# Kernel tuning notes

Hardware: AMD Instinct MI355X
Metric: run time of the kernel (lower is better)

## Reference

```python
import jax, jax.numpy as jnp
import numpy as np


def _conv3x3_relu(x, w, b):
    # 3x3 conv, padding 1 (SAME), NCHW / OIHW, then ReLU (Conv2d with activation=ReLU)
    y = jax.lax.conv_general_dilated(x, w, (1, 1), ((1, 1), (1, 1)),
                                     dimension_numbers=('NCHW', 'OIHW', 'NCHW'))
    return jax.nn.relu(y + b[None, :, None, None])


def _forward(features, cnn_w, cnn_b, gcn_w, gcn_b, up_w, up_b,
             deconv_w, deconv_b, pred_w, pred_b):
    # ---- CNN stack (mask_fcn1..4) ----
    x = features
    for i in range(cnn_w.shape[0]):
        x = _conv3x3_relu(x, cnn_w[i], cnn_b[i])

    B, C, H, W = x.shape
    N = H * W  # pixels = graph nodes per ROI

    # ---- cosine-similarity adjacency per sample ----
    f = x.reshape(B, C, N).transpose(0, 2, 1)          # [B, N, C] node features
    norms = jnp.linalg.norm(f, axis=-1, keepdims=True)
    fn = f / jnp.maximum(norms, 1e-8)
    A = jnp.einsum('bnc,bmc->bnm', fn, fn)             # [B, N, N]

    # ---- symmetric GCN normalization with self-loops: D^-1/2 (A+I) D^-1/2 ----
    A = A + jnp.eye(N, dtype=A.dtype)[None]
    d = jnp.sum(A, axis=-1)                            # [B, N]
    dinv = jax.lax.rsqrt(jnp.maximum(d, 1e-12))
    A = A * dinv[:, :, None] * dinv[:, None, :]

    # ---- GCN layers: x' = A_hat @ (x W) + b, then GELU ----
    g = f
    for i in range(gcn_w.shape[0]):
        g = jnp.einsum('bnm,bmc->bnc', A, g @ gcn_w[i]) + gcn_b[i]
        g = jax.nn.gelu(g, approximate=False)

    x = g.transpose(0, 2, 1).reshape(B, C, H, W)

    # ---- Upsample head ----
    for i in range(up_w.shape[0]):
        x = _conv3x3_relu(x, up_w[i], up_b[i])
    feats = x  # returned roi_features, [B, C, H, W]

    # ConvTranspose2d(k=2, s=2): dilated conv with flipped, IO-swapped kernel
    wt = jnp.flip(deconv_w, (2, 3)).transpose(1, 0, 2, 3)  # (out, in, 2, 2)
    y = jax.lax.conv_general_dilated(feats, wt, (1, 1), ((1, 1), (1, 1)),
                                     lhs_dilation=(2, 2),
                                     dimension_numbers=('NCHW', 'OIHW', 'NCHW'))
    y = jax.nn.relu(y + deconv_b[None, :, None, None])    # [B, C, 2H, 2W]

    mask = jax.lax.conv_general_dilated(y, pred_w, (1, 1), ((0, 0), (0, 0)),
                                        dimension_numbers=('NCHW', 'OIHW', 'NCHW'))
    mask = mask + pred_b[None, :, None, None]             # [B, num_classes, 2H, 2W]
    return mask, feats


def setup_inputs() -> dict:
    key = jax.random.key(0)
    ks = jax.random.split(key, 12)
    B, C, H, W, NC = 512, 256, 14, 14, 80

    def p(k, shape, s=0.05):
        return jax.random.normal(k, shape, jnp.float32) * s

    return {
        'features': jax.random.normal(ks[0], (B, C, H, W), jnp.float32),
        'cnn_w': p(ks[1], (4, C, C, 3, 3)),
        'cnn_b': p(ks[2], (4, C)),
        'gcn_w': p(ks[3], (2, C, C)),
        'gcn_b': p(ks[4], (2, C)),
        'up_w': p(ks[5], (2, C, C, 3, 3)),
        'up_b': p(ks[6], (2, C)),
        'deconv_w': p(ks[7], (C, C, 2, 2)),  # PyTorch ConvTranspose2d layout (in, out, kH, kW)
        'deconv_b': p(ks[8], (C,)),
        'pred_w': p(ks[9], (NC, C, 1, 1)),
        'pred_b': p(ks[10], (NC,)),
    }


def reference(features, cnn_w, cnn_b, gcn_w, gcn_b, up_w, up_b,
              deconv_w, deconv_b, pred_w, pred_b):
    return _forward(features, cnn_w, cnn_b, gcn_w, gcn_b, up_w, up_b,
                    deconv_w, deconv_b, pred_w, pred_b)
```

## Files before the change

### kernel.cpp

```cpp
#include <hip/hip_runtime.h>
#include <stdint.h>

typedef __attribute__((ext_vector_type(8))) short short8;
typedef __attribute__((ext_vector_type(4))) float f32x4;

#define B_N   512
#define NPIX  196
#define MTOT  (B_N*NPIX)
#define NPAD  224

static_assert(MTOT % 128 == 0, "M must tile by 128");

__device__ __forceinline__ float bf2f(unsigned short u){
  unsigned int x = ((unsigned int)u) << 16;
  return __builtin_bit_cast(float, x);
}
__device__ __forceinline__ unsigned short f2bf(float f){
  unsigned int x = __builtin_bit_cast(unsigned int, f);
  x += 0x7fffu + ((x >> 16) & 1u);
  return (unsigned short)(x >> 16);
}
__device__ __forceinline__ void gload16(const void* g, void* l){
  __builtin_amdgcn_global_load_lds(
    (const __attribute__((address_space(1))) void*)(uintptr_t)g,
    (__attribute__((address_space(3))) void*)(uintptr_t)l, 16, 0, 0);
}
__device__ __forceinline__ float gelu_exact(float x){
  return 0.5f * x * (1.f + erff(x * 0.70710678118654752440f));
}

template<int EPI>
__global__ __launch_bounds__(256, 3) void gemm_conv(
    const unsigned short* __restrict__ A, const unsigned short* __restrict__ Bt,
    unsigned short* __restrict__ outb, float* __restrict__ outf,
    const float* __restrict__ bias)
{
  __shared__ __align__(16) char smem[2*10240 + 64];
  const int tid = threadIdx.x;
  const int wid = tid >> 6, lane = tid & 63;
  const int wr = wid >> 1, wc = wid & 1;
  const int orig = blockIdx.x;
  const int vid = (orig & 7) * 196 + (orig >> 3);
  const int m0 = (vid >> 1) * 128;
  const int nb = vid & 1;

  const int ssw = ((lane & 3) ^ ((lane >> 3) & 3)) << 4;
  const int s16 = (lane >> 4) << 4;

  if (tid < 16) ((int*)(smem + 20480))[tid] = 0;

  auto stageA = [&](int cc, char* dst){
#pragma unroll
    for (int s = 0; s < 3; ++s) {
      const int g = wid + s*4;
      if (g < 10) {
        const int r = g*16 + (lane >> 2);
        long gr = (long)m0 - 16 + r;
        if (gr < 0) gr = 0;
        if (gr >= MTOT) gr = MTOT - 1;
        gload16((const char*)A + (size_t)gr*512 + (size_t)cc*64 + (size_t)ssw,
                dst + g*1024);
      }
    }
  };

  f32x4 acc[4][4];
#pragma unroll
  for (int i=0;i<4;i++)
#pragma unroll
    for (int j=0;j<4;j++) acc[i][j] = (f32x4){0.f,0.f,0.f,0.f};

  int arow[4]; unsigned hh[4], ww[4];
#pragma unroll
  for (int i=0;i<4;i++){
    const int ml = wr*64 + i*16 + (lane&15);
    arow[i] = ml + 16;
    const int p = (m0 + ml) % NPIX;
    hh[i] = (unsigned)(p / 14); ww[i] = (unsigned)(p % 14);
  }

  const unsigned short* bbase = Bt + ((size_t)(nb*8 + wc*4)*64 + lane)*8;
  const char* pz = smem + 20480 + s16;

  stageA(0, smem);
  __syncthreads();

#pragma unroll 1
  for (int c = 0; c < 8; ++c) {
    if (c < 7) stageA(c+1, smem + ((c+1)&1)*10240);
    const char* aB = smem + (c&1)*10240;
#pragma unroll 3
    for (int tap = 0; tap < 9; ++tap) {
      const unsigned short* bp = bbase + (size_t)(tap*8 + c)*8192;
      short8 bv[4];
#pragma unroll
      for (int j=0;j<4;j++) bv[j] = *(const short8*)(bp + j*512);
      const int dh = tap/3 - 1, dw = tap - (tap/3)*3 - 1;
      const int doff = dh*14 + dw;
      short8 av[4];
#pragma unroll
      for (int i=0;i<4;i++){
        const int r = arow[i] + doff;
        const char* pa = aB + r*64 + (s16 ^ (((r>>1)&3)<<4));
        const bool val = (hh[i] + (unsigned)dh < 14u) && (ww[i] + (unsigned)dw < 14u);
        av[i] = *(const short8*)(val ? pa : pz);
      }
#pragma unroll
      for (int i=0;i<4;i++)
#pragma unroll
        for (int j=0;j<4;j++)
          acc[i][j] = __builtin_amdgcn_mfma_f32_16x16x32_bf16(av[i], bv[j], acc[i][j], 0,0,0);
    }
    __syncthreads();
  }

#pragma unroll
  for (int i=0;i<4;i++){
#pragma unroll
    for (int j=0;j<4;j++){
#pragma unroll
      for (int r=0;r<4;r++){
        const int row = m0 + wr*64 + i*16 + ((lane>>4)<<2) + r;
        const int col = nb*128 + wc*64 + j*16 + (lane&15);
        float v = acc[i][j][r] + bias[col];
        v = fmaxf(v, 0.f);
        outb[(size_t)row*256 + col] = f2bf(v);
        if constexpr (EPI == 1) {
          const int b = row / NPIX, p = row - b*NPIX;
          outf[((size_t)b*256 + col)*NPIX + p] = v;
        }
      }
    }
  }
}

__global__ __launch_bounds__(512) void k_decpred(
    const unsigned short* __restrict__ A, const unsigned short* __restrict__ Bdec,
    const unsigned short* __restrict__ Bpred, const float* __restrict__ decb,
    const float* __restrict__ predb, float* __restrict__ mask)
{
  __shared__ __align__(16) char smem[49152];
  char* sA = smem;
  char* sD = smem + 32768;
  const int tid = threadIdx.x;
  const int wid = tid >> 6, lane = tid & 63;
  const int m0 = blockIdx.x * 64;
  const int ssw = ((lane & 3) ^ ((lane >> 3) & 3)) << 4;
  const int s16 = (lane >> 4) << 4;
  const int wr = wid >> 2, wn = wid & 3;

#pragma unroll
  for (int p = 0; p < 4; ++p) {
    const int cc = p*2 + (wid >> 2);
    const int r  = (wid & 3)*16 + (lane >> 2);
    gload16((const char*)A + (size_t)(m0 + r)*512 + (size_t)cc*64 + (size_t)ssw,
            sA + cc*4096 + (wid & 3)*1024);
  }

  float bd[4];
#pragma unroll
  for (int j = 0; j < 4; ++j) bd[j] = decb[wn*64 + j*16 + (lane & 15)];
  float pb[2]; int pcol[2];
#pragma unroll
  for (int j = 0; j < 2; ++j) {
    pcol[j] = wn*32 + j*16 + (lane & 15);
    pb[j] = (pcol[j] < 80) ? predb[pcol[j]] : 0.f;
  }

  __syncthreads();

#pragma unroll 1
  for (int tap = 0; tap < 4; ++tap) {
    f32x4 acc[2][4];
#pragma unroll
    for (int i=0;i<2;i++)
#pragma unroll
      for (int j=0;j<4;j++) acc[i][j] = (f32x4){0.f,0.f,0.f,0.f};
#pragma unroll
    for (int c = 0; c < 8; ++c) {
      short8 bv[4];
#pragma unroll
      for (int j=0;j<4;j++)
        bv[j] = *(const short8*)(Bdec + (size_t)((tap*8+c)*16 + wn*4+j)*512 + lane*8);
      short8 av[2];
#pragma unroll
      for (int i=0;i<2;i++){
        const int rA = wr*32 + i*16 + (lane&15);
        av[i] = *(const short8*)(sA + c*4096 + rA*64 + (s16 ^ (((rA>>1)&3)<<4)));
      }
#pragma unroll
      for (int i=0;i<2;i++)
#pragma unroll
        for (int j=0;j<4;j++)
          acc[i][j] = __builtin_amdgcn_mfma_f32_16x16x32_bf16(av[i], bv[j], acc[i][j],0,0,0);
    }

    f32x4 acc2[2][2];
#pragma unroll
    for (int i=0;i<2;i++)
#pragma unroll
      for (int j=0;j<2;j++) acc2[i][j] = (f32x4){0.f,0.f,0.f,0.f};

#pragma unroll 1
    for (int h = 0; h < 2; ++h) {
      if ((wn >> 1) == h) {
#pragma unroll
        for (int i=0;i<2;i++)
#pragma unroll
          for (int j=0;j<4;j++)
#pragma unroll
            for (int rr=0;rr<4;rr++){
              const int row = wr*32 + i*16 + ((lane>>4)<<2) + rr;
              const int colL = (wn&1)*64 + j*16 + (lane&15);
              const float v = fmaxf(acc[i][j][rr] + bd[j], 0.f);
              *(unsigned short*)(sD + row*256 + (((colL>>3) ^ (row&7))<<4)
                                 + ((colL<<1)&15)) = f2bf(v);
            }
      }
      __syncthreads();
#pragma unroll
      for (int c = 0; c < 4; ++c) {
        short8 bp2[2];
#pragma unroll
        for (int j=0;j<2;j++)
          bp2[j] = *(const short8*)(Bpred + (size_t)((h*4+c)*8 + wn*2+j)*512 + lane*8);
        short8 ap[2];
#pragma unroll
        for (int i=0;i<2;i++){
          const int rP = wr*32 + i*16 + (lane&15);
          ap[i] = *(const short8*)(sD + rP*256 + (((c*4 + (lane>>4)) ^ (rP&7))<<4));
        }
#pragma unroll
        for (int i=0;i<2;i++)
#pragma unroll
          for (int j=0;j<2;j++)
            acc2[i][j] = __builtin_amdgcn_mfma_f32_16x16x32_bf16(ap[i], bp2[j], acc2[i][j],0,0,0);
      }
      __syncthreads();
    }
#pragma unroll
    for (int i=0;i<2;i++)
#pragma unroll
      for (int j=0;j<2;j++)
#pragma unroll
        for (int rr=0;rr<4;rr++){
          if (pcol[j] < 80) {
            const int row = m0 + wr*32 + i*16 + ((lane>>4)<<2) + rr;
            const int b = row / NPIX, p = row - b*NPIX;
            const int hh = p/14, ww2 = p - hh*14;
            mask[(((size_t)b*80 + pcol[j])*28 + 2*hh + (tap>>1))*28 + 2*ww2 + (tap&1)]
                = acc2[i][j][rr] + pb[j];
          }
        }
  }
}

template<int KI, int EPI>
__global__ __launch_bounds__(256) void gemm_g(
    const unsigned short* __restrict__ A, const unsigned short* __restrict__ Bt,
    unsigned short* __restrict__ outb, float* __restrict__ outf,
    const float* __restrict__ bias, int th, int tw)
{
  __shared__ __align__(16) char smem[16384];
  char* sA = smem; char* sB = smem + 8192;
  const int tid = threadIdx.x;
  const int wid = tid >> 6, lane = tid & 63;
  const int wr = wid >> 1, wc = wid & 1;
  const int m0 = blockIdx.x * 128, n0 = blockIdx.y * 128;
  const int rs = wid*16 + (lane >> 2);
  const int ssw = ((lane & 3) ^ ((lane >> 3) & 3)) << 4;
  char* dA0 = sA + wid*1024; char* dA1 = sA + 4096 + wid*1024;
  char* dB0 = sB + wid*1024; char* dB1 = sB + 4096 + wid*1024;
  const char* pA0 = (const char*)(A + (size_t)(m0 + rs)      * (KI*32));
  const char* pA1 = (const char*)(A + (size_t)(m0 + rs + 64) * (KI*32));
  const char* pB0 = (const char*)(Bt + (size_t)(n0 + rs)      * (KI*32));
  const char* pB1 = (const char*)(Bt + (size_t)(n0 + rs + 64) * (KI*32));

  f32x4 acc[4][4];
#pragma unroll
  for (int i=0;i<4;i++)
#pragma unroll
    for (int j=0;j<4;j++) acc[i][j] = (f32x4){0.f,0.f,0.f,0.f};

  const int s16 = (lane >> 4) << 4;

#pragma unroll 1
  for (int kk = 0; kk < KI; ++kk) {
    const int ko = kk*64 + ssw;
    gload16(pA0 + ko, dA0);
    gload16(pA1 + ko, dA1);
    gload16(pB0 + ko, dB0);
    gload16(pB1 + ko, dB1);
    __syncthreads();
    short8 av[4], bv[4];
#pragma unroll
    for (int i=0;i<4;i++){
      const int ra = wr*64 + i*16 + (lane&15);
      const int rb = wc*64 + i*16 + (lane&15);
      av[i] = *(const short8*)(sA + ra*64 + (s16 ^ (((ra>>1)&3)<<4)));
      bv[i] = *(const short8*)(sB + rb*64 + (s16 ^ (((rb>>1)&3)<<4)));
    }
#pragma unroll
    for (int i=0;i<4;i++)
#pragma unroll
      for (int j=0;j<4;j++)
        acc[i][j] = __builtin_amdgcn_mfma_f32_16x16x32_bf16(av[i], bv[j], acc[i][j], 0,0,0);
    __syncthreads();
  }

#pragma unroll
  for (int i=0;i<4;i++){
#pragma unroll
    for (int j=0;j<4;j++){
#pragma unroll
      for (int r=0;r<4;r++){
        const int row = m0 + wr*64 + i*16 + ((lane>>4)<<2) + r;
        const int col = n0 + wc*64 + j*16 + (lane&15);
        float v = acc[i][j][r];
        if constexpr (EPI == 0) {
          v += bias[col];
          v = fmaxf(v, 0.f);
          outb[(size_t)row*256 + col] = f2bf(v);
        } else if constexpr (EPI == 2) {
          const int b = row / NPIX, p = row - b*NPIX;
          outb[((size_t)b*256 + col)*NPAD + p] = f2bf(v);
        }
      }
    }
  }
}

template<int EPI, int KI>
__global__ __launch_bounds__(256) void gemm_s(
    const unsigned short* __restrict__ Asrc, int a_rps, int a_stride, long amax,
    const unsigned short* __restrict__ Bsrc, int b_rps, int b_stride, long bmax,
    unsigned short* __restrict__ outb, const float* __restrict__ bias)
{
  __shared__ __align__(16) char smem[16384];
  char* sA = smem; char* sB = smem + 8192;
  const int tid = threadIdx.x;
  const int wid = tid >> 6, lane = tid & 63;
  const int wr = wid >> 1, wc = wid & 1;
  const int m0 = blockIdx.x * 128, n0 = blockIdx.y * 128;
  const int b  = blockIdx.z;
  const int rs = wid*16 + (lane >> 2);
  const int ssw = ((lane & 3) ^ ((lane >> 3) & 3)) << 4;
  char* dA0 = sA + wid*1024; char* dA1 = sA + 4096 + wid*1024;
  char* dB0 = sB + wid*1024; char* dB1 = sB + 4096 + wid*1024;
  long ar0 = (long)b*a_rps + m0 + rs;       if (ar0 > amax) ar0 = amax;
  long ar1 = (long)b*a_rps + m0 + rs + 64;  if (ar1 > amax) ar1 = amax;
  long br0 = (long)b*b_rps + n0 + rs;       if (br0 > bmax) br0 = bmax;
  long br1 = (long)b*b_rps + n0 + rs + 64;  if (br1 > bmax) br1 = bmax;
  const char* pA0  = (const char*)(Asrc + ar0 * a_stride);
  const char* pA1  = (const char*)(Asrc + ar1 * a_stride);
  const char* pBt0 = (const char*)(Bsrc + br0 * b_stride);
  const char* pBt1 = (const char*)(Bsrc + br1 * b_stride);

  f32x4 acc[4][4];
#pragma unroll
  for (int i=0;i<4;i++)
#pragma unroll
    for (int j=0;j<4;j++) acc[i][j] = (f32x4){0.f,0.f,0.f,0.f};

  const int s16 = (lane >> 4) << 4;

#pragma unroll 1
  for (int kk = 0; kk < KI; ++kk) {
    const int ko = kk*64 + ssw;
    gload16(pA0 + ko, dA0);
    gload16(pA1 + ko, dA1);
    gload16(pBt0 + ko, dB0);
    gload16(pBt1 + ko, dB1);
    __syncthreads();
    short8 av[4], bv[4];
#pragma unroll
    for (int i=0;i<4;i++){
      const int ra = wr*64 + i*16 + (lane&15);
      const int rb = wc*64 + i*16 + (lane&15);
      av[i] = *(const short8*)(sA + ra*64 + (s16 ^ (((ra>>1)&3)<<4)));
      bv[i] = *(const short8*)(sB + rb*64 + (s16 ^ (((rb>>1)&3)<<4)));
    }
#pragma unroll
    for (int i=0;i<4;i++)
#pragma unroll
      for (int j=0;j<4;j++)
        acc[i][j] = __builtin_amdgcn_mfma_f32_16x16x32_bf16(av[i], bv[j], acc[i][j], 0,0,0);
    __syncthreads();
  }

  if constexpr (EPI == 4) {
    int nlv[4]; float dn[4];
#pragma unroll
    for (int j=0;j<4;j++){
      nlv[j] = n0 + wc*64 + j*16 + (lane&15);
      dn[j] = (nlv[j] < NPIX) ? bias[(size_t)b*NPIX + nlv[j]] : 0.f;
    }
#pragma unroll
    for (int i=0;i<4;i++){
#pragma unroll
      for (int r=0;r<4;r++){
        const int ml = m0 + wr*64 + i*16 + ((lane>>4)<<2) + r;
        const float dmv = (ml < NPIX) ? bias[(size_t)b*NPIX + ml] : 0.f;
        if (ml < NPAD) {
#pragma unroll
          for (int j=0;j<4;j++){
            if (nlv[j] < NPAD) {
              const float o = (acc[i][j][r] + ((ml==nlv[j]) ? 1.f : 0.f)) * dmv * dn[j];
              outb[((size_t)b*NPAD + ml)*NPAD + nlv[j]] = f2bf(o);
            }
          }
        }
      }
    }
  } else {
#pragma unroll
    for (int i=0;i<4;i++){
#pragma unroll
      for (int j=0;j<4;j++){
#pragma unroll
        for (int r=0;r<4;r++){
          const int ml = m0 + wr*64 + i*16 + ((lane>>4)<<2) + r;
          const int nl = n0 + wc*64 + j*16 + (lane&15);
          if (ml < NPIX) {
            const float x = acc[i][j][r] + bias[nl];
            outb[((size_t)b*NPIX + ml)*256 + nl] = f2bf(gelu_exact(x));
          }
        }
      }
    }
  }
}


__global__ void k_tin(const float* __restrict__ in, unsigned short* __restrict__ out)
{
  __shared__ float t[32][29];
  const int b = blockIdx.x, p0 = blockIdx.y * 28, c0 = blockIdx.z * 32;
  const int tid = threadIdx.x;
  for (int i = tid; i < 896; i += 256) {
    const int c = i / 28, p = i - c*28;
    t[c][p] = in[((size_t)b*256 + c0 + c)*196 + p0 + p];
  }
  __syncthreads();
  for (int i = tid; i < 896; i += 256) {
    const int p = i >> 5, c = i & 31;
    out[((size_t)b*196 + p0 + p)*256 + c0 + c] = f2bf(t[c][p]);
  }
}

__global__ void k_fnnorm(const unsigned short* __restrict__ f, unsigned short* __restrict__ fn)
{
  const int row  = blockIdx.x * 4 + (threadIdx.x >> 6);
  const int lane = threadIdx.x & 63;
  const unsigned short* src = f + (size_t)row*256 + lane*4;
  const float x0 = bf2f(src[0]), x1 = bf2f(src[1]), x2 = bf2f(src[2]), x3 = bf2f(src[3]);
  float s = x0*x0 + x1*x1 + x2*x2 + x3*x3;
#pragma unroll
  for (int o = 32; o > 0; o >>= 1) s += __shfl_xor(s, o, 64);
  const float scale = 1.f / fmaxf(sqrtf(s), 1e-8f);
  unsigned short* dst = fn + (size_t)row*256 + lane*4;
  dst[0]=f2bf(x0*scale); dst[1]=f2bf(x1*scale); dst[2]=f2bf(x2*scale); dst[3]=f2bf(x3*scale);
}

__global__ void k_ssum(const unsigned short* __restrict__ fn, float* __restrict__ S)
{
  const int b = blockIdx.x, c = threadIdx.x;
  const unsigned short* p = fn + (size_t)b*NPIX*256 + c;
  float s = 0.f;
  for (int i = 0; i < NPIX; ++i) s += bf2f(p[(size_t)i*256]);
  S[b*256 + c] = s;
}

__global__ void k_dinv(const unsigned short* __restrict__ fn, const float* __restrict__ S,
                       float* __restrict__ dinv)
{
  const int row  = blockIdx.x * 4 + (threadIdx.x >> 6);
  const int lane = threadIdx.x & 63;
  const int b = row / NPIX;
  const unsigned short* p = fn + (size_t)row*256 + lane*4;
  const float* sp = S + b*256 + lane*4;
  float d = bf2f(p[0])*sp[0] + bf2f(p[1])*sp[1] + bf2f(p[2])*sp[2] + bf2f(p[3])*sp[3];
#pragma unroll
  for (int o = 32; o > 0; o >>= 1) d += __shfl_xor(d, o, 64);
  if (lane == 0) dinv[row] = rsqrtf(fmaxf(d + 1.f, 1e-12f));
}

__global__ void k_prep(const float* __restrict__ cnn_w, const float* __restrict__ up_w,
                       const float* __restrict__ gcn_w, const float* __restrict__ dec_w,
                       const float* __restrict__ pred_w,
                       unsigned short* __restrict__ bt_cnn, unsigned short* __restrict__ bt_up,
                       unsigned short* __restrict__ bt_gcn, unsigned short* __restrict__ bt_dec,
                       unsigned short* __restrict__ bt_pred, unsigned short* __restrict__ tcm)
{
  long i = (long)blockIdx.x * 256 + threadIdx.x;
  long n = 4L*589824;
  if (i < n) {
    const long l = i / 589824, r = i % 589824;
    const long tap = r >> 16, r2 = r & 65535;
    const long c = r2 >> 13, n16 = (r2 >> 9) & 15, kchunk = (r2 >> 7) & 3;
    const long nl = (r2 >> 3) & 15, ke = r2 & 7;
    const long co = n16*16 + nl, ci = c*32 + kchunk*8 + ke;
    bt_cnn[i] = f2bf(cnn_w[(((l*256+co)*256+ci)*3 + tap/3)*3 + (tap%3)]);
    return;
  }
  i -= n; n = 2L*589824;
  if (i < n) {
    const long l = i / 589824, r = i % 589824;
    const long tap = r >> 16, r2 = r & 65535;
    const long c = r2 >> 13, n16 = (r2 >> 9) & 15, kchunk = (r2 >> 7) & 3;
    const long nl = (r2 >> 3) & 15, ke = r2 & 7;
    const long co = n16*16 + nl, ci = c*32 + kchunk*8 + ke;
    bt_up[i] = f2bf(up_w[(((l*256+co)*256+ci)*3 + tap/3)*3 + (tap%3)]);
    return;
  }
  i -= n; n = 2L*256*256;
  if (i < n) {
    const long ci = i & 255, co = (i >> 8) & 255, l = i >> 16;
    bt_gcn[i] = f2bf(gcn_w[(l*256 + ci)*256 + co]);
    return;
  }
  i -= n; n = 262144;
  if (i < n) {
    const long ke = i&7, nl = (i>>3)&15, k4 = (i>>7)&3, g = (i>>9)&15;
    const long c = (i>>13)&7, tap = i>>16;
    const long co = g*16 + nl, ci = c*32 + k4*8 + ke;
    bt_dec[i] = f2bf(dec_w[((ci*256 + co)*2 + (tap>>1))*2 + (tap&1)]);
    return;
  }
  i -= n; n = 32768;
  if (i < n) {
    const long ke = i&7, nl = (i>>3)&15, k4 = (i>>7)&3, g = (i>>9)&7, c = i>>12;
    const long cls = g*16 + nl, ci = c*32 + k4*8 + ke;
    bt_pred[i] = (cls < 80) ? f2bf(pred_w[cls*256 + ci]) : (unsigned short)0;
    return;
  }
  i -= n; n = 512L*256*28;
  if (i < n) {
    const long p = 196 + (i % 28);
    const long rest = i / 28;
    const long c = rest & 255, bb = rest >> 8;
    tcm[((size_t)(bb*256 + c))*NPAD + p] = 0;
    return;
  }
}

extern "C" void kernel_launch(void* const* d_in, const int* in_sizes, int n_in,
                              void* d_out, int out_size, void* d_ws, size_t ws_size,
                              hipStream_t stream)
{
  const float* features = (const float*)d_in[0];
  const float* cnn_w  = (const float*)d_in[1];
  const float* cnn_b  = (const float*)d_in[2];
  const float* gcn_w  = (const float*)d_in[3];
  const float* gcn_b  = (const float*)d_in[4];
  const float* up_w   = (const float*)d_in[5];
  const float* up_b   = (const float*)d_in[6];
  const float* dec_w  = (const float*)d_in[7];
  const float* dec_b  = (const float*)d_in[8];
  const float* pred_w = (const float*)d_in[9];
  const float* pred_b = (const float*)d_in[10];

  char* ws = (char*)d_ws;
  size_t o = 0;
  auto take = [&](size_t nbytes) -> char* {
    char* p = ws + o;
    o += (nbytes + 255) & ~(size_t)255;
    return p;
  };
  unsigned short* bt_cnn  = (unsigned short*)take(4L*589824*2);
  unsigned short* bt_up   = (unsigned short*)take(2L*589824*2);
  unsigned short* bt_gcn  = (unsigned short*)take(2L*256*256*2);
  unsigned short* bt_dec  = (unsigned short*)take(262144L*2);
  unsigned short* bt_pred = (unsigned short*)take(32768L*2);
  unsigned short* actA    = (unsigned short*)take((size_t)MTOT*256*2);
  unsigned short* actB    = (unsigned short*)take((size_t)MTOT*256*2);
  unsigned short* ahat    = (unsigned short*)take((size_t)B_N*NPAD*NPAD*2);
  unsigned short* tcm     = (unsigned short*)take((size_t)B_N*256*NPAD*2);
  float*          Sbuf    = (float*)take((size_t)B_N*256*4);
  float*          dinvb   = (float*)take((size_t)MTOT*4);

  float* mask  = (float*)d_out;
  float* feats = mask + (size_t)B_N*80*28*28;

  const dim3 blk(256);
  const dim3 gc(1568);
  const dim3 gg(MTOT/128, 2);
  const dim3 gs(2, 2, B_N);

  k_prep<<<29824, blk, 0, stream>>>(cnn_w, up_w, gcn_w, dec_w, pred_w,
                                    bt_cnn, bt_up, bt_gcn, bt_dec, bt_pred, tcm);
  k_tin<<<dim3(B_N, 7, 8), blk, 0, stream>>>(features, actA);

  gemm_conv<0><<<gc, blk, 0, stream>>>(actA, bt_cnn + 0L*589824, actB, nullptr, cnn_b + 0);
  gemm_conv<0><<<gc, blk, 0, stream>>>(actB, bt_cnn + 1L*589824, actA, nullptr, cnn_b + 256);
  gemm_conv<0><<<gc, blk, 0, stream>>>(actA, bt_cnn + 2L*589824, actB, nullptr, cnn_b + 512);
  gemm_conv<0><<<gc, blk, 0, stream>>>(actB, bt_cnn + 3L*589824, actA, nullptr, cnn_b + 768);

  k_fnnorm<<<MTOT/4, blk, 0, stream>>>(actA, actB);
  k_ssum<<<B_N, blk, 0, stream>>>(actB, Sbuf);
  k_dinv<<<MTOT/4, blk, 0, stream>>>(actB, Sbuf, dinvb);
  gemm_s<4,8><<<gs, blk, 0, stream>>>(actB, NPIX, 256, (long)MTOT-1,
                                      actB, NPIX, 256, (long)MTOT-1, ahat, dinvb);

  gemm_g<8,2><<<gg, blk, 0, stream>>>(actA, bt_gcn, tcm, nullptr, nullptr, 0,0);
  gemm_s<5,7><<<gs, blk, 0, stream>>>(ahat, NPAD, NPAD, (long)B_N*NPAD-1,
                                      tcm, 256, NPAD, (long)B_N*256-1, actB, gcn_b);
  gemm_g<8,2><<<gg, blk, 0, stream>>>(actB, bt_gcn + 65536, tcm, nullptr, nullptr, 0,0);
  gemm_s<5,7><<<gs, blk, 0, stream>>>(ahat, NPAD, NPAD, (long)B_N*NPAD-1,
                                      tcm, 256, NPAD, (long)B_N*256-1, actA, gcn_b + 256);

  gemm_conv<0><<<gc, blk, 0, stream>>>(actA, bt_up + 0L*589824, actB, nullptr, up_b + 0);
  gemm_conv<1><<<gc, blk, 0, stream>>>(actB, bt_up + 1L*589824, actA, feats,   up_b + 256);

  k_decpred<<<dim3(MTOT/64), dim3(512), 0, stream>>>(actA, bt_dec, bt_pred,
                                                     dec_b, pred_b, mask);
}
```

Baseline: 1.455 ms.

## Register-staged padded A tiles in conv GEMM; widen and pair taps in decpred

The 3x3 conv GEMM now loads its A tile into registers and writes it to LDS after computing, instead of using async global-to-LDS copies. It uses an 80-byte padded row stride in place of the XOR swizzle, precomputes per-tap validity bitmasks, fully unrolls the tap loop, and skips the final barrier. The deconv+pred kernel now writes the full 256-column deconv output into a wider LDS tile and runs the 1x1 pred GEMM in one pass instead of two halves. It also processes horizontal tap pairs together so mask stores become float2 writes. The risks are higher register pressure from staging and full unroll, and more LDS per block, which can reduce occupancy.

```diff
diff --git a/kernel.cpp b/kernel.cpp
--- a/kernel.cpp
+++ b/kernel.cpp
@@ -35,7 +35,7 @@
     unsigned short* __restrict__ outb, float* __restrict__ outf,
     const float* __restrict__ bias)
 {
-  __shared__ __align__(16) char smem[2*10240 + 64];
+  __shared__ __align__(16) char smem[2*12800 + 2560];
   const int tid = threadIdx.x;
   const int wid = tid >> 6, lane = tid & 63;
   const int wr = wid >> 1, wc = wid & 1;
@@ -44,25 +44,38 @@
   const int m0 = (vid >> 1) * 128;
   const int nb = vid & 1;
 
-  const int ssw = ((lane & 3) ^ ((lane >> 3) & 3)) << 4;
   const int s16 = (lane >> 4) << 4;
 
-  if (tid < 16) ((int*)(smem + 20480))[tid] = 0;
-
-  auto stageA = [&](int cc, char* dst){
-#pragma unroll
-    for (int s = 0; s < 3; ++s) {
-      const int g = wid + s*4;
-      if (g < 10) {
-        const int r = g*16 + (lane >> 2);
-        long gr = (long)m0 - 16 + r;
-        if (gr < 0) gr = 0;
-        if (gr >= MTOT) gr = MTOT - 1;
-        gload16((const char*)A + (size_t)gr*512 + (size_t)cc*64 + (size_t)ssw,
-                dst + g*1024);
-      }
-    }
+  for (int z = tid; z < 640; z += 256) ((int*)(smem + 25600))[z] = 0;
+
+  const int r0 = (wid    )*16 + (lane >> 2);
+  const int r1 = (wid + 4)*16 + (lane >> 2);
+  const int r2 = (wid + 8)*16 + (lane >> 2);
+  auto clampr = [&](int r)->long{
+    long gr = (long)m0 - 16 + r;
+    if (gr < 0) gr = 0;
+    if (gr >= MTOT) gr = MTOT - 1;
+    return gr;
   };
+  const char* gsrc0 = (const char*)A + clampr(r0)*512 + (lane&3)*16;
+  const char* gsrc1 = (const char*)A + clampr(r1)*512 + (lane&3)*16;
+  const char* gsrc2 = (const char*)A + clampr(r2)*512 + (lane&3)*16;
+  const int loff0 = r0*80 + (lane&3)*16;
+  const int loff1 = r1*80 + (lane&3)*16;
+  const int loff2 = r2*80 + (lane&3)*16;
+
+  short8 stg0, stg1, stg2;
+  auto loadA = [&](int cc){
+    stg0 = *(const short8*)(gsrc0 + cc*64);
+    stg1 = *(const short8*)(gsrc1 + cc*64);
+    if (wid < 2) stg2 = *(const short8*)(gsrc2 + cc*64);
+  };
+  auto writeA = [&](int buf){
+    char* base = smem + buf*12800;
+    *(short8*)(base + loff0) = stg0;
+    *(short8*)(base + loff1) = stg1;
+    if (wid < 2) *(short8*)(base + loff2) = stg2;
+  };
 
   f32x4 acc[4][4];
 #pragma unroll
@@ -70,48 +83,60 @@
 #pragma unroll
     for (int j=0;j<4;j++) acc[i][j] = (f32x4){0.f,0.f,0.f,0.f};
 
-  int arow[4]; unsigned hh[4], ww[4];
+  const char* abase[4]; int vmask[4];
 #pragma unroll
   for (int i=0;i<4;i++){
     const int ml = wr*64 + i*16 + (lane&15);
-    arow[i] = ml + 16;
+    const int arow = ml + 16;
+    abase[i] = smem + (arow - 15)*80 + s16;
     const int p = (m0 + ml) % NPIX;
-    hh[i] = (unsigned)(p / 14); ww[i] = (unsigned)(p % 14);
-  }
+    const int hh = p / 14, ww = p - hh*14;
+    int m = 0;
+#pragma unroll
+    for (int tap = 0; tap < 9; ++tap){
+      const int dh = tap/3 - 1, dw = tap - (tap/3)*3 - 1;
+      const bool val = ((unsigned)(hh + dh) < 14u) && ((unsigned)(ww + dw) < 14u);
+      m |= (val ? 1 : 0) << tap;
+    }
+    vmask[i] = m;
+  }
+  const char* pzb = smem + 25600 + s16;
 
   const unsigned short* bbase = Bt + ((size_t)(nb*8 + wc*4)*64 + lane)*8;
-  const char* pz = smem + 20480 + s16;
-
-  stageA(0, smem);
+
+  loadA(0);
+  writeA(0);
   __syncthreads();
 
 #pragma unroll 1
   for (int c = 0; c < 8; ++c) {
-    if (c < 7) stageA(c+1, smem + ((c+1)&1)*10240);
-    const char* aB = smem + (c&1)*10240;
-#pragma unroll 3
+    if (c < 7) loadA(c+1);
+    const int abuf = (c & 1) * 12800;
+    const char* a0 = abase[0] + abuf;
+    const char* a1 = abase[1] + abuf;
+    const char* a2 = abase[2] + abuf;
+    const char* a3 = abase[3] + abuf;
+#pragma unroll
     for (int tap = 0; tap < 9; ++tap) {
       const unsigned short* bp = bbase + (size_t)(tap*8 + c)*8192;
       short8 bv[4];
 #pragma unroll
       for (int j=0;j<4;j++) bv[j] = *(const short8*)(bp + j*512);
       const int dh = tap/3 - 1, dw = tap - (tap/3)*3 - 1;
-      const int doff = dh*14 + dw;
+      const int koff = ((dh*14 + dw) + 15) * 80;
       short8 av[4];
-#pragma unroll
-      for (int i=0;i<4;i++){
-        const int r = arow[i] + doff;
-        const char* pa = aB + r*64 + (s16 ^ (((r>>1)&3)<<4));
-        const bool val = (hh[i] + (unsigned)dh < 14u) && (ww[i] + (unsigned)dw < 14u);
-        av[i] = *(const short8*)(val ? pa : pz);
-      }
+      av[0] = *(const short8*)(((vmask[0] >> tap) & 1) ? a0 + koff : pzb + koff);
+      av[1] = *(const short8*)(((vmask[1] >> tap) & 1) ? a1 + koff : pzb + koff);
+      av[2] = *(const short8*)(((vmask[2] >> tap) & 1) ? a2 + koff : pzb + koff);
+      av[3] = *(const short8*)(((vmask[3] >> tap) & 1) ? a3 + koff : pzb + koff);
 #pragma unroll
       for (int i=0;i<4;i++)
 #pragma unroll
         for (int j=0;j<4;j++)
           acc[i][j] = __builtin_amdgcn_mfma_f32_16x16x32_bf16(av[i], bv[j], acc[i][j], 0,0,0);
     }
-    __syncthreads();
+    if (c < 7) writeA((c+1)&1);
+    if (c < 7) __syncthreads();
   }
 
 #pragma unroll
@@ -139,7 +164,7 @@
     const unsigned short* __restrict__ Bpred, const float* __restrict__ decb,
     const float* __restrict__ predb, float* __restrict__ mask)
 {
-  __shared__ __align__(16) char smem[49152];
+  __shared__ __align__(16) char smem[65536];
   char* sA = smem;
   char* sD = smem + 32768;
   const int tid = threadIdx.x;
@@ -170,88 +195,87 @@
   __syncthreads();
 
 #pragma unroll 1
-  for (int tap = 0; tap < 4; ++tap) {
-    f32x4 acc[2][4];
-#pragma unroll
-    for (int i=0;i<2;i++)
-#pragma unroll
-      for (int j=0;j<4;j++) acc[i][j] = (f32x4){0.f,0.f,0.f,0.f};
-#pragma unroll
-    for (int c = 0; c < 8; ++c) {
-      short8 bv[4];
-#pragma unroll
-      for (int j=0;j<4;j++)
-        bv[j] = *(const short8*)(Bdec + (size_t)((tap*8+c)*16 + wn*4+j)*512 + lane*8);
-      short8 av[2];
-#pragma unroll
-      for (int i=0;i<2;i++){
-        const int rA = wr*32 + i*16 + (lane&15);
-        av[i] = *(const short8*)(sA + c*4096 + rA*64 + (s16 ^ (((rA>>1)&3)<<4)));
+  for (int th = 0; th < 2; ++th) {
+    f32x4 accP[2][2][2];
+#pragma unroll
+    for (int tw = 0; tw < 2; ++tw) {
+      const int tap = th*2 + tw;
+      f32x4 acc[2][4];
+#pragma unroll
+      for (int i=0;i<2;i++)
+#pragma unroll
+        for (int j=0;j<4;j++) acc[i][j] = (f32x4){0.f,0.f,0.f,0.f};
+#pragma unroll
+      for (int c = 0; c < 8; ++c) {
+        short8 bv[4];
+#pragma unroll
+        for (int j=0;j<4;j++)
+          bv[j] = *(const short8*)(Bdec + (size_t)((tap*8+c)*16 + wn*4+j)*512 + lane*8);
+        short8 av[2];
+#pragma unroll
+        for (int i=0;i<2;i++){
+          const int rA = wr*32 + i*16 + (lane&15);
+          av[i] = *(const short8*)(sA + c*4096 + rA*64 + (s16 ^ (((rA>>1)&3)<<4)));
+        }
+#pragma unroll
+        for (int i=0;i<2;i++)
+#pragma unroll
+          for (int j=0;j<4;j++)
+            acc[i][j] = __builtin_amdgcn_mfma_f32_16x16x32_bf16(av[i], bv[j], acc[i][j],0,0,0);
       }
 #pragma unroll
       for (int i=0;i<2;i++)
 #pragma unroll
         for (int j=0;j<4;j++)
-          acc[i][j] = __builtin_amdgcn_mfma_f32_16x16x32_bf16(av[i], bv[j], acc[i][j],0,0,0);
-    }
-
-    f32x4 acc2[2][2];
-#pragma unroll
-    for (int i=0;i<2;i++)
-#pragma unroll
-      for (int j=0;j<2;j++) acc2[i][j] = (f32x4){0.f,0.f,0.f,0.f};
-
-#pragma unroll 1
-    for (int h = 0; h < 2; ++h) {
-      if ((wn >> 1) == h) {
+#pragma unroll
+          for (int rr=0;rr<4;rr++){
+            const int row = wr*32 + i*16 + ((lane>>4)<<2) + rr;
+            const int colL = wn*64 + j*16 + (lane&15);
+            const float v = fmaxf(acc[i][j][rr] + bd[j], 0.f);
+            *(unsigned short*)(sD + row*512 + ((colL<<1) ^ ((row&7)<<4))) = f2bf(v);
+          }
+      __syncthreads();
+#pragma unroll
+      for (int i=0;i<2;i++)
+#pragma unroll
+        for (int j=0;j<2;j++) accP[tw][i][j] = (f32x4){0.f,0.f,0.f,0.f};
+#pragma unroll
+      for (int c = 0; c < 8; ++c) {
+        short8 bp2[2];
+#pragma unroll
+        for (int j=0;j<2;j++)
+          bp2[j] = *(const short8*)(Bpred + (size_t)(c*8 + wn*2+j)*512 + lane*8);
+        short8 ap[2];
+#pragma unroll
+        for (int i=0;i<2;i++){
+          const int rP = wr*32 + i*16 + (lane&15);
+          ap[i] = *(const short8*)(sD + rP*512 + ((c*64 + s16) ^ ((rP&7)<<4)));
+        }
 #pragma unroll
         for (int i=0;i<2;i++)
 #pragma unroll
-          for (int j=0;j<4;j++)
-#pragma unroll
-            for (int rr=0;rr<4;rr++){
-              const int row = wr*32 + i*16 + ((lane>>4)<<2) + rr;
-              const int colL = (wn&1)*64 + j*16 + (lane&15);
-              const float v = fmaxf(acc[i][j][rr] + bd[j], 0.f);
-              *(unsigned short*)(sD + row*256 + (((colL>>3) ^ (row&7))<<4)
-                                 + ((colL<<1)&15)) = f2bf(v);
-            }
+          for (int j=0;j<2;j++)
+            accP[tw][i][j] = __builtin_amdgcn_mfma_f32_16x16x32_bf16(ap[i], bp2[j], accP[tw][i][j],0,0,0);
       }
       __syncthreads();
-#pragma unroll
-      for (int c = 0; c < 4; ++c) {
-        short8 bp2[2];
-#pragma unroll
-        for (int j=0;j<2;j++)
-          bp2[j] = *(const short8*)(Bpred + (size_t)((h*4+c)*8 + wn*2+j)*512 + lane*8);
-        short8 ap[2];
-#pragma unroll
-        for (int i=0;i<2;i++){
-          const int rP = wr*32 + i*16 + (lane&15);
-          ap[i] = *(const short8*)(sD + rP*256 + (((c*4 + (lane>>4)) ^ (rP&7))<<4));
-        }
-#pragma unroll
-        for (int i=0;i<2;i++)
-#pragma unroll
-          for (int j=0;j<2;j++)
-            acc2[i][j] = __builtin_amdgcn_mfma_f32_16x16x32_bf16(ap[i], bp2[j], acc2[i][j],0,0,0);
-      }
-      __syncthreads();
     }
 #pragma unroll
     for (int i=0;i<2;i++)
 #pragma unroll
-      for (int j=0;j<2;j++)
-#pragma unroll
-        for (int rr=0;rr<4;rr++){
-          if (pcol[j] < 80) {
+      for (int j=0;j<2;j++){
+        if (pcol[j] < 80) {
+#pragma unroll
+          for (int rr=0;rr<4;rr++){
             const int row = m0 + wr*32 + i*16 + ((lane>>4)<<2) + rr;
             const int b = row / NPIX, p = row - b*NPIX;
-            const int hh = p/14, ww2 = p - hh*14;
-            mask[(((size_t)b*80 + pcol[j])*28 + 2*hh + (tap>>1))*28 + 2*ww2 + (tap&1)]
-                = acc2[i][j][rr] + pb[j];
+            const int hh = p/14, w2 = p - hh*14;
+            float2 v2;
+            v2.x = accP[0][i][j][rr] + pb[j];
+            v2.y = accP[1][i][j][rr] + pb[j];
+            *(float2*)&mask[(((size_t)b*80 + pcol[j])*28 + 2*hh + th)*28 + 2*w2] = v2;
           }
         }
+      }
   }
 }
 
```

Measured after the change: 1.485 ms. 2.0% more time.

## Widen conv tiles to full 256 columns and pair deconv taps for float2 mask stores

Applied to the files above, without the earlier changes.

The implicit-GEMM conv kernel now uses 512-thread blocks that cover all 256 output channels for a 128-row tile. This halves the grid and means each staged A tile (with halo) is loaded once instead of twice. The decpred kernel now processes tap pairs along the width and keeps all 256 deconv channels in a larger 64KB shared buffer. That lets the pred GEMM run over the full K in one pass and write adjacent mask pixels as float2. The cost is more registers and LDS per block, which may lower occupancy.

```diff
diff --git a/kernel.cpp b/kernel.cpp
--- a/kernel.cpp
+++ b/kernel.cpp
@@ -30,7 +30,7 @@
 }
 
 template<int EPI>
-__global__ __launch_bounds__(256, 3) void gemm_conv(
+__global__ __launch_bounds__(512, 4) void gemm_conv(
     const unsigned short* __restrict__ A, const unsigned short* __restrict__ Bt,
     unsigned short* __restrict__ outb, float* __restrict__ outf,
     const float* __restrict__ bias)
@@ -38,11 +38,10 @@
   __shared__ __align__(16) char smem[2*10240 + 64];
   const int tid = threadIdx.x;
   const int wid = tid >> 6, lane = tid & 63;
-  const int wr = wid >> 1, wc = wid & 1;
+  const int wr = wid >> 2, wn = wid & 3;
   const int orig = blockIdx.x;
-  const int vid = (orig & 7) * 196 + (orig >> 3);
-  const int m0 = (vid >> 1) * 128;
-  const int nb = vid & 1;
+  const int vid = (orig & 7) * 98 + (orig >> 3);
+  const int m0 = vid * 128;
 
   const int ssw = ((lane & 3) ^ ((lane >> 3) & 3)) << 4;
   const int s16 = (lane >> 4) << 4;
@@ -51,8 +50,8 @@
 
   auto stageA = [&](int cc, char* dst){
 #pragma unroll
-    for (int s = 0; s < 3; ++s) {
-      const int g = wid + s*4;
+    for (int s = 0; s < 2; ++s) {
+      const int g = wid + s*8;
       if (g < 10) {
         const int r = g*16 + (lane >> 2);
         long gr = (long)m0 - 16 + r;
@@ -79,7 +78,7 @@
     hh[i] = (unsigned)(p / 14); ww[i] = (unsigned)(p % 14);
   }
 
-  const unsigned short* bbase = Bt + ((size_t)(nb*8 + wc*4)*64 + lane)*8;
+  const unsigned short* bbase = Bt + ((size_t)(wn*4)*64 + lane)*8;
   const char* pz = smem + 20480 + s16;
 
   stageA(0, smem);
@@ -121,7 +120,7 @@
 #pragma unroll
       for (int r=0;r<4;r++){
         const int row = m0 + wr*64 + i*16 + ((lane>>4)<<2) + r;
-        const int col = nb*128 + wc*64 + j*16 + (lane&15);
+        const int col = wn*64 + j*16 + (lane&15);
         float v = acc[i][j][r] + bias[col];
         v = fmaxf(v, 0.f);
         outb[(size_t)row*256 + col] = f2bf(v);
@@ -139,7 +138,7 @@
     const unsigned short* __restrict__ Bpred, const float* __restrict__ decb,
     const float* __restrict__ predb, float* __restrict__ mask)
 {
-  __shared__ __align__(16) char smem[49152];
+  __shared__ __align__(16) char smem[65536];
   char* sA = smem;
   char* sD = smem + 32768;
   const int tid = threadIdx.x;
@@ -170,88 +169,87 @@
   __syncthreads();
 
 #pragma unroll 1
-  for (int tap = 0; tap < 4; ++tap) {
-    f32x4 acc[2][4];
-#pragma unroll
-    for (int i=0;i<2;i++)
-#pragma unroll
-      for (int j=0;j<4;j++) acc[i][j] = (f32x4){0.f,0.f,0.f,0.f};
-#pragma unroll
-    for (int c = 0; c < 8; ++c) {
-      short8 bv[4];
-#pragma unroll
-      for (int j=0;j<4;j++)
-        bv[j] = *(const short8*)(Bdec + (size_t)((tap*8+c)*16 + wn*4+j)*512 + lane*8);
-      short8 av[2];
-#pragma unroll
-      for (int i=0;i<2;i++){
-        const int rA = wr*32 + i*16 + (lane&15);
-        av[i] = *(const short8*)(sA + c*4096 + rA*64 + (s16 ^ (((rA>>1)&3)<<4)));
-      }
+  for (int th = 0; th < 2; ++th) {
+    f32x4 accP[2][2][2];
+#pragma unroll
+    for (int tw = 0; tw < 2; ++tw) {
+      const int tap = th*2 + tw;
+      f32x4 acc[2][4];
 #pragma unroll
       for (int i=0;i<2;i++)
 #pragma unroll
+        for (int j=0;j<4;j++) acc[i][j] = (f32x4){0.f,0.f,0.f,0.f};
+#pragma unroll
+      for (int c = 0; c < 8; ++c) {
+        short8 bv[4];
+#pragma unroll
         for (int j=0;j<4;j++)
-          acc[i][j] = __builtin_amdgcn_mfma_f32_16x16x32_bf16(av[i], bv[j], acc[i][j],0,0,0);
-    }
-
-    f32x4 acc2[2][2];
-#pragma unroll
-    for (int i=0;i<2;i++)
-#pragma unroll
-      for (int j=0;j<2;j++) acc2[i][j] = (f32x4){0.f,0.f,0.f,0.f};
-
-#pragma unroll 1
-    for (int h = 0; h < 2; ++h) {
-      if ((wn >> 1) == h) {
+          bv[j] = *(const short8*)(Bdec + (size_t)((tap*8+c)*16 + wn*4+j)*512 + lane*8);
+        short8 av[2];
+#pragma unroll
+        for (int i=0;i<2;i++){
+          const int rA = wr*32 + i*16 + (lane&15);
+          av[i] = *(const short8*)(sA + c*4096 + rA*64 + (s16 ^ (((rA>>1)&3)<<4)));
+        }
 #pragma unroll
         for (int i=0;i<2;i++)
 #pragma unroll
           for (int j=0;j<4;j++)
-#pragma unroll
-            for (int rr=0;rr<4;rr++){
-              const int row = wr*32 + i*16 + ((lane>>4)<<2) + rr;
-              const int colL = (wn&1)*64 + j*16 + (lane&15);
-              const float v = fmaxf(acc[i][j][rr] + bd[j], 0.f);
-              *(unsigned short*)(sD + row*256 + (((colL>>3) ^ (row&7))<<4)
-                                 + ((colL<<1)&15)) = f2bf(v);
-            }
-      }
+            acc[i][j] = __builtin_amdgcn_mfma_f32_16x16x32_bf16(av[i], bv[j], acc[i][j],0,0,0);
+      }
+#pragma unroll
+      for (int i=0;i<2;i++)
+#pragma unroll
+        for (int j=0;j<4;j++)
+#pragma unroll
+          for (int rr=0;rr<4;rr++){
+            const int row = wr*32 + i*16 + ((lane>>4)<<2) + rr;
+            const int colL = wn*64 + j*16 + (lane&15);
+            const float v = fmaxf(acc[i][j][rr] + bd[j], 0.f);
+            *(unsigned short*)(sD + row*512 + ((colL<<1) ^ ((row&7)<<4))) = f2bf(v);
+          }
       __syncthreads();
 #pragma unroll
-      for (int c = 0; c < 4; ++c) {
+      for (int i=0;i<2;i++)
+#pragma unroll
+        for (int j=0;j<2;j++) accP[tw][i][j] = (f32x4){0.f,0.f,0.f,0.f};
+#pragma unroll
+      for (int c = 0; c < 8; ++c) {
         short8 bp2[2];
 #pragma unroll
         for (int j=0;j<2;j++)
-          bp2[j] = *(const short8*)(Bpred + (size_t)((h*4+c)*8 + wn*2+j)*512 + lane*8);
+          bp2[j] = *(const short8*)(Bpred + (size_t)(c*8 + wn*2+j)*512 + lane*8);
         short8 ap[2];
 #pragma unroll
         for (int i=0;i<2;i++){
           const int rP = wr*32 + i*16 + (lane&15);
-          ap[i] = *(const short8*)(sD + rP*256 + (((c*4 + (lane>>4)) ^ (rP&7))<<4));
+          ap[i] = *(const short8*)(sD + rP*512 + ((c*64 + s16) ^ ((rP&7)<<4)));
         }
 #pragma unroll
         for (int i=0;i<2;i++)
 #pragma unroll
           for (int j=0;j<2;j++)
-            acc2[i][j] = __builtin_amdgcn_mfma_f32_16x16x32_bf16(ap[i], bp2[j], acc2[i][j],0,0,0);
+            accP[tw][i][j] = __builtin_amdgcn_mfma_f32_16x16x32_bf16(ap[i], bp2[j], accP[tw][i][j],0,0,0);
       }
       __syncthreads();
     }
 #pragma unroll
     for (int i=0;i<2;i++)
 #pragma unroll
-      for (int j=0;j<2;j++)
-#pragma unroll
-        for (int rr=0;rr<4;rr++){
-          if (pcol[j] < 80) {
+      for (int j=0;j<2;j++){
+        if (pcol[j] < 80) {
+#pragma unroll
+          for (int rr=0;rr<4;rr++){
             const int row = m0 + wr*32 + i*16 + ((lane>>4)<<2) + rr;
             const int b = row / NPIX, p = row - b*NPIX;
-            const int hh = p/14, ww2 = p - hh*14;
-            mask[(((size_t)b*80 + pcol[j])*28 + 2*hh + (tap>>1))*28 + 2*ww2 + (tap&1)]
-                = acc2[i][j][rr] + pb[j];
+            const int hh = p/14, w2 = p - hh*14;
+            float2 v2;
+            v2.x = accP[0][i][j][rr] + pb[j];
+            v2.y = accP[1][i][j][rr] + pb[j];
+            *(float2*)&mask[(((size_t)b*80 + pcol[j])*28 + 2*hh + th)*28 + 2*w2] = v2;
           }
         }
+      }
   }
 }
 
@@ -583,7 +581,7 @@
   float* feats = mask + (size_t)B_N*80*28*28;
 
   const dim3 blk(256);
-  const dim3 gc(1568);
+  const dim3 gc(784);
   const dim3 gg(MTOT/128, 2);
   const dim3 gs(2, 2, B_N);
 
@@ -591,10 +589,10 @@
                                     bt_cnn, bt_up, bt_gcn, bt_dec, bt_pred, tcm);
   k_tin<<<dim3(B_N, 7, 8), blk, 0, stream>>>(features, actA);
 
-  gemm_conv<0><<<gc, blk, 0, stream>>>(actA, bt_cnn + 0L*589824, actB, nullptr, cnn_b + 0);
-  gemm_conv<0><<<gc, blk, 0, stream>>>(actB, bt_cnn + 1L*589824, actA, nullptr, cnn_b + 256);
-  gemm_conv<0><<<gc, blk, 0, stream>>>(actA, bt_cnn + 2L*589824, actB, nullptr, cnn_b + 512);
-  gemm_conv<0><<<gc, blk, 0, stream>>>(actB, bt_cnn + 3L*589824, actA, nullptr, cnn_b + 768);
+  gemm_conv<0><<<gc, dim3(512), 0, stream>>>(actA, bt_cnn + 0L*589824, actB, nullptr, cnn_b + 0);
+  gemm_conv<0><<<gc, dim3(512), 0, stream>>>(actB, bt_cnn + 1L*589824, actA, nullptr, cnn_b + 256);
+  gemm_conv<0><<<gc, dim3(512), 0, stream>>>(actA, bt_cnn + 2L*589824, actB, nullptr, cnn_b + 512);
+  gemm_conv<0><<<gc, dim3(512), 0, stream>>>(actB, bt_cnn + 3L*589824, actA, nullptr, cnn_b + 768);
 
   k_fnnorm<<<MTOT/4, blk, 0, stream>>>(actA, actB);
   k_ssum<<<B_N, blk, 0, stream>>>(actB, Sbuf);
@@ -609,8 +607,8 @@
   gemm_s<5,7><<<gs, blk, 0, stream>>>(ahat, NPAD, NPAD, (long)B_N*NPAD-1,
                                       tcm, 256, NPAD, (long)B_N*256-1, actA, gcn_b + 256);
 
-  gemm_conv<0><<<gc, blk, 0, stream>>>(actA, bt_up + 0L*589824, actB, nullptr, up_b + 0);
-  gemm_conv<1><<<gc, blk, 0, stream>>>(actB, bt_up + 1L*589824, actA, feats,   up_b + 256);
+  gemm_conv<0><<<gc, dim3(512), 0, stream>>>(actA, bt_up + 0L*589824, actB, nullptr, up_b + 0);
+  gemm_conv<1><<<gc, dim3(512), 0, stream>>>(actB, bt_up + 1L*589824, actA, feats,   up_b + 256);
 
   k_decpred<<<dim3(MTOT/64), dim3(512), 0, stream>>>(actA, bt_dec, bt_pred,
                                                      dec_b, pred_b, mask);
```

New measurement: 1.436 ms (median of 2 runs). Within noise of the previous version (-1.3%).
